# Kernel optimization log

Measured on AMD Instinct MI355X. Metric: run time of the kernel, lower is better.

Reference implementation:

```python
import jax, jax.numpy as jnp
import numpy as np

N, E = 50000, 800000
C, H, EC = 64, 3, 32  # node_channels, heads, edge_channels
NEG_SLOPE = 0.2


def _kaiming(key, shape, fan_in):
    bound = np.sqrt(6.0 / fan_in)  # kaiming_uniform_ default (a=sqrt(5)-ish approx; gain sqrt(2) variant)
    return jax.random.uniform(key, shape, jnp.float32, -bound, bound)


def setup_inputs() -> dict:
    key = jax.random.key(0)
    ks = jax.random.split(key, 8)
    x = jax.random.normal(ks[0], (N, C), jnp.float32)
    edge_index = jax.random.randint(ks[1], (2, E), 0, N, jnp.int64)
    edge_attr = jax.random.normal(ks[2], (E, EC), jnp.float32)
    weight_node = _kaiming(ks[3], (C, H * C), C)
    weight_edge = _kaiming(ks[4], (EC, H * C), EC)
    weight_triplet_att = _kaiming(ks[5], (1, H, 3 * C), 3 * C)
    weight_scale = _kaiming(ks[6], (H * C, C), H * C)
    bias = jnp.zeros((C,), jnp.float32)
    return {"x": x, "edge_index": edge_index, "edge_attr": edge_attr,
            "weight_node": weight_node, "weight_edge": weight_edge,
            "weight_triplet_att": weight_triplet_att,
            "weight_scale": weight_scale, "bias": bias}


def reference(x, edge_index, edge_attr, weight_node, weight_edge,
              weight_triplet_att, weight_scale, bias):
    src = edge_index[0]  # j (source)
    dst = edge_index[1]  # i (target), PyG default flow source_to_target

    xp = x @ weight_node                     # [N, H*C]
    ep = edge_attr @ weight_edge             # [E, H*C]

    x_j = xp[src].reshape(E, H, C)
    x_i = xp[dst].reshape(E, H, C)
    e_ij = ep.reshape(E, H, C)

    # attention weight split along concat order [x_i, e_ij, x_j]
    w = weight_triplet_att.reshape(H, 3, C)
    alpha = (jnp.einsum('ehc,hc->eh', x_i, w[:, 0])
             + jnp.einsum('ehc,hc->eh', e_ij, w[:, 1])
             + jnp.einsum('ehc,hc->eh', x_j, w[:, 2]))   # [E, H]
    alpha = jnp.where(alpha >= 0, alpha, NEG_SLOPE * alpha)  # leaky_relu

    # segment softmax over destination nodes (PyG softmax semantics)
    seg_max = jax.ops.segment_max(alpha, dst, num_segments=N)    # [N, H]
    alpha = jnp.exp(alpha - seg_max[dst])
    seg_sum = jax.ops.segment_sum(alpha, dst, num_segments=N)    # [N, H]
    alpha = alpha / (seg_sum[dst] + 1e-16)

    msg = alpha[:, :, None] * e_ij * x_j                         # [E, H, C]
    aggr = jax.ops.segment_sum(msg.reshape(E, H * C), dst, num_segments=N)  # [N, H*C]

    return aggr @ weight_scale + bias                            # [N, C]
```

## Files before the change

kernel.cpp:

```cpp
#include <hip/hip_runtime.h>

#define CC    64
#define HH    3
#define ECC   32
#define HCdim 192
#define NEG_SLOPE 0.2f
#define ASHIFT 12.0f

typedef float v2f __attribute__((ext_vector_type(2)));

__global__ void tm_k0(const float* __restrict__ We, const float* __restrict__ wt,
                      float* __restrict__ u) {
    int t = threadIdx.x;
    if (t >= HH * ECC) return;
    int h = t >> 5, k = t & 31;
    float s = 0.f;
    #pragma unroll
    for (int c = 0; c < CC; ++c)
        s = fmaf(We[k * HCdim + h * CC + c], wt[h * HCdim + CC + c], s);
    u[t] = s;
}

#define K1_ROWS 64
__global__ __launch_bounds__(192) void tm_k1(const float* __restrict__ x,
        const float* __restrict__ Wn, const float* __restrict__ wt,
        const int* __restrict__ ei, int* __restrict__ deg,
        float* __restrict__ xp, float* __restrict__ sA, int N, int E) {
    __shared__ float wl[CC * HCdim];
    __shared__ float xl[K1_ROWS * CC];
    const int t = threadIdx.x;
    for (int i = blockIdx.x * 192 + t; i < E; i += gridDim.x * 192)
        atomicAdd(&deg[ei[E + i]], 1);
    const int h = t >> 6, c = t & 63;
    {
        float4* wl4 = (float4*)wl;
        const float4* Wn4 = (const float4*)Wn;
        for (int i = t; i < CC * HCdim / 4; i += 192) wl4[i] = Wn4[i];
    }
    const int base = blockIdx.x * K1_ROWS;
    const int rows = min(K1_ROWS, N - base);
    {
        float4* xl4 = (float4*)xl;
        const float4* x4 = (const float4*)(x + (size_t)base * CC);
        for (int i = t; i < rows * CC / 4; i += 192) xl4[i] = x4[i];
    }
    const float w0c = wt[h * HCdim + c];
    const float w2c = wt[h * HCdim + 2 * CC + c];
    __syncthreads();
    for (int rt = 0; rt < rows; rt += 4) {
        float acc0 = 0.f, acc1 = 0.f, acc2 = 0.f, acc3 = 0.f;
        #pragma unroll 4
        for (int k = 0; k < CC; k += 4) {
            const float w0  = wl[(k + 0) * HCdim + t];
            const float w1  = wl[(k + 1) * HCdim + t];
            const float w2_ = wl[(k + 2) * HCdim + t];
            const float w3  = wl[(k + 3) * HCdim + t];
            const float4 xa = *(const float4*)&xl[(rt + 0) * CC + k];
            const float4 xb = *(const float4*)&xl[(rt + 1) * CC + k];
            const float4 xc = *(const float4*)&xl[(rt + 2) * CC + k];
            const float4 xd = *(const float4*)&xl[(rt + 3) * CC + k];
            acc0 = fmaf(xa.x, w0, fmaf(xa.y, w1, fmaf(xa.z, w2_, fmaf(xa.w, w3, acc0))));
            acc1 = fmaf(xb.x, w0, fmaf(xb.y, w1, fmaf(xb.z, w2_, fmaf(xb.w, w3, acc1))));
            acc2 = fmaf(xc.x, w0, fmaf(xc.y, w1, fmaf(xc.z, w2_, fmaf(xc.w, w3, acc2))));
            acc3 = fmaf(xd.x, w0, fmaf(xd.y, w1, fmaf(xd.z, w2_, fmaf(xd.w, w3, acc3))));
        }
        #pragma unroll
        for (int r = 0; r < 4; ++r) {
            const float v = (r == 0) ? acc0 : (r == 1) ? acc1 : (r == 2) ? acc2 : acc3;
            const int n = base + rt + r;
            xp[(size_t)n * HCdim + t] = v;
            float a0 = v * w0c, a2 = v * w2c;
            #pragma unroll
            for (int o = 32; o; o >>= 1) {
                a0 += __shfl_xor(a0, o);
                a2 += __shfl_xor(a2, o);
            }
            if (c == 0) {
                sA[n * 8 + h]     = a0;
                sA[n * 8 + 4 + h] = a2;
            }
        }
    }
}

__global__ __launch_bounds__(256) void tm_scanA(const int* __restrict__ deg,
        int* __restrict__ bsum, int N) {
    __shared__ int sd[256];
    int t = threadIdx.x, n = blockIdx.x * 256 + t;
    sd[t] = (n < N) ? deg[n] : 0;
    __syncthreads();
    for (int o = 128; o; o >>= 1) {
        if (t < o) sd[t] += sd[t + o];
        __syncthreads();
    }
    if (!t) bsum[blockIdx.x] = sd[0];
}

__global__ __launch_bounds__(256) void tm_scanB(const int* __restrict__ bsum,
        int* __restrict__ boff, int nb) {
    __shared__ int sd[256];
    int t = threadIdx.x;
    int v = (t < nb) ? bsum[t] : 0;
    sd[t] = v;
    __syncthreads();
    for (int o = 1; o < 256; o <<= 1) {
        int x = (t >= o) ? sd[t - o] : 0;
        __syncthreads();
        sd[t] += x;
        __syncthreads();
    }
    if (t < nb) boff[t] = sd[t] - v;
}

__global__ __launch_bounds__(256) void tm_scanC(const int* __restrict__ deg,
        const int* __restrict__ boff, int* __restrict__ off,
        int* __restrict__ cursor, int N) {
    __shared__ int sd[256];
    int t = threadIdx.x, n = blockIdx.x * 256 + t;
    int v = (n < N) ? deg[n] : 0;
    sd[t] = v;
    __syncthreads();
    for (int o = 1; o < 256; o <<= 1) {
        int x = (t >= o) ? sd[t - o] : 0;
        __syncthreads();
        sd[t] += x;
        __syncthreads();
    }
    if (n < N) {
        int ex = boff[blockIdx.x] + sd[t] - v;
        off[n] = ex;
        cursor[n] = ex;
        if (n == N - 1) off[N] = ex + v;
    }
}

__global__ __launch_bounds__(256) void tm_alpha(const int* __restrict__ ei,
        const float* __restrict__ ea, const float* __restrict__ u,
        const float* __restrict__ sA, int* __restrict__ cursor,
        float4* __restrict__ alphaE, int2* __restrict__ perm, int E) {
    __shared__ float ul[HH * ECC];
    const int t = threadIdx.x;
    if (t < HH * ECC) ul[t] = u[t];
    __syncthreads();
    const int e = blockIdx.x * 256 + t;
    if (e >= E) return;
    const int src = ei[e];
    const int dst = ei[E + e];
    float av[ECC];
    const float4* p4 = (const float4*)(ea + (size_t)e * ECC);
    #pragma unroll
    for (int q = 0; q < 8; ++q) {
        float4 v = p4[q];
        av[4*q] = v.x; av[4*q+1] = v.y; av[4*q+2] = v.z; av[4*q+3] = v.w;
    }
    float d0 = 0.f, d1 = 0.f, d2 = 0.f;
    #pragma unroll
    for (int k = 0; k < ECC; ++k) {
        d0 = fmaf(av[k], ul[k], d0);
        d1 = fmaf(av[k], ul[ECC + k], d1);
        d2 = fmaf(av[k], ul[2 * ECC + k], d2);
    }
    const float4 s0 = *(const float4*)(sA + (size_t)dst * 8);
    const float4 s2 = *(const float4*)(sA + (size_t)src * 8 + 4);
    float a0 = s0.x + d0 + s2.x;
    float a1 = s0.y + d1 + s2.y;
    float a2 = s0.z + d2 + s2.z;
    a0 = (a0 >= 0.f) ? a0 : NEG_SLOPE * a0;
    a1 = (a1 >= 0.f) ? a1 : NEG_SLOPE * a1;
    a2 = (a2 >= 0.f) ? a2 : NEG_SLOPE * a2;
    alphaE[e] = make_float4(a0, a1, a2, 0.f);
    const int pos = atomicAdd(&cursor[dst], 1);
    perm[pos] = make_int2(src * (HCdim * 4), e * (ECC * 4));
}

__global__ __launch_bounds__(192) void tm_agg(const int2* __restrict__ perm,
        const int* __restrict__ off, const float* __restrict__ ea,
        const float* __restrict__ We, const float* __restrict__ alphaE,
        const float* __restrict__ xp, float* __restrict__ aggrN, int N) {
    const int t = threadIdx.x;
    const int h = t >> 6, lane = t & 63;
    const char* __restrict__ ea_b = (const char*)ea;
    const char* __restrict__ xp_b = (const char*)xp;
    const char* __restrict__ al_b = (const char*)alphaE;
    v2f wcol2[16];
    #pragma unroll
    for (int k2 = 0; k2 < 16; ++k2) {
        wcol2[k2].x = We[(2 * k2)     * HCdim + h * CC + lane];
        wcol2[k2].y = We[(2 * k2 + 1) * HCdim + h * CC + lane];
    }
    const int xoff = h * CC * 4 + lane * 4;
    const int aoff = h * 4;
    for (int n = blockIdx.x; n < N; n += gridDim.x) {
        const int start = off[n], end = off[n + 1];
        float s = 0.f, acc = 0.f;
        int pos = start;
        for (; pos + 2 <= end; pos += 2) {
            const int4 pp = *(const int4*)&perm[pos];
            const int so0 = __builtin_amdgcn_readfirstlane(pp.x);
            const int eo0 = __builtin_amdgcn_readfirstlane(pp.y);
            const int so1 = __builtin_amdgcn_readfirstlane(pp.z);
            const int eo1 = __builtin_amdgcn_readfirstlane(pp.w);
            const float a0 = *(const float*)(al_b + (eo0 >> 3) + aoff);
            const float a1 = *(const float*)(al_b + (eo1 >> 3) + aoff);
            const float4* q0 = (const float4*)(ea_b + eo0);
            const float4* q1 = (const float4*)(ea_b + eo1);
            const float xj0 = *(const float*)(xp_b + so0 + xoff);
            const float xj1 = *(const float*)(xp_b + so1 + xoff);
            v2f d0 = {0.f, 0.f}, d1 = {0.f, 0.f};
            #pragma unroll
            for (int q = 0; q < 8; ++q) {
                const float4 v0 = q0[q];
                const float4 v1 = q1[q];
                const v2f wlo = wcol2[2 * q], whi = wcol2[2 * q + 1];
                d0 = (v2f){v0.x, v0.y} * wlo + d0;
                d0 = (v2f){v0.z, v0.w} * whi + d0;
                d1 = (v2f){v1.x, v1.y} * wlo + d1;
                d1 = (v2f){v1.z, v1.w} * whi + d1;
            }
            const float p0 = __expf(a0 - ASHIFT);
            const float p1 = __expf(a1 - ASHIFT);
            s += p0 + p1;
            acc = fmaf(p0 * (d0.x + d0.y), xj0, acc);
            acc = fmaf(p1 * (d1.x + d1.y), xj1, acc);
        }
        if (pos < end) {
            const int2 pe = perm[pos];
            const int so = __builtin_amdgcn_readfirstlane(pe.x);
            const int eo = __builtin_amdgcn_readfirstlane(pe.y);
            const float a = *(const float*)(al_b + (eo >> 3) + aoff);
            const float4* q4 = (const float4*)(ea_b + eo);
            const float xj = *(const float*)(xp_b + so + xoff);
            v2f d = {0.f, 0.f};
            #pragma unroll
            for (int q = 0; q < 8; ++q) {
                const float4 v = q4[q];
                d = (v2f){v.x, v.y} * wcol2[2 * q]     + d;
                d = (v2f){v.z, v.w} * wcol2[2 * q + 1] + d;
            }
            const float p = __expf(a - ASHIFT);
            s += p;
            acc = fmaf(p * (d.x + d.y), xj, acc);
        }
        aggrN[(size_t)n * HCdim + h * CC + lane] = acc / (s + 1e-16f);
    }
}

#define K5_ROWS 16
__global__ __launch_bounds__(256) void tm_k5(const float* __restrict__ aggrN,
        const float* __restrict__ Ws, const float* __restrict__ bias,
        float* __restrict__ out, int N) {
    __shared__ float wsl[HCdim * CC];
    __shared__ float al[K5_ROWS * HCdim];
    const int t = threadIdx.x;
    const int part = t >> 6, c = t & 63;
    {
        float4* w4 = (float4*)wsl;
        const float4* Ws4 = (const float4*)Ws;
        for (int i = t; i < HCdim * CC / 4; i += 256) w4[i] = Ws4[i];
    }
    const float b = bias[c];
    const int base = blockIdx.x * K5_ROWS;
    const int rows = min(K5_ROWS, N - base);
    {
        float4* al4 = (float4*)al;
        const float4* a4 = (const float4*)(aggrN + (size_t)base * HCdim);
        for (int i = t; i < rows * HCdim / 4; i += 256) al4[i] = a4[i];
    }
    __syncthreads();
    const int r0 = part * 4;
    if (r0 >= rows) return;
    float acc0 = b, acc1 = b, acc2 = b, acc3 = b;
    #pragma unroll 4
    for (int k = 0; k < HCdim; k += 4) {
        const float w0  = wsl[(k + 0) * CC + c];
        const float w1  = wsl[(k + 1) * CC + c];
        const float w2_ = wsl[(k + 2) * CC + c];
        const float w3  = wsl[(k + 3) * CC + c];
        const float4 xa = *(const float4*)&al[(r0 + 0) * HCdim + k];
        const float4 xb = *(const float4*)&al[(r0 + 1) * HCdim + k];
        const float4 xc = *(const float4*)&al[(r0 + 2) * HCdim + k];
        const float4 xd = *(const float4*)&al[(r0 + 3) * HCdim + k];
        acc0 = fmaf(xa.x, w0, fmaf(xa.y, w1, fmaf(xa.z, w2_, fmaf(xa.w, w3, acc0))));
        acc1 = fmaf(xb.x, w0, fmaf(xb.y, w1, fmaf(xb.z, w2_, fmaf(xb.w, w3, acc1))));
        acc2 = fmaf(xc.x, w0, fmaf(xc.y, w1, fmaf(xc.z, w2_, fmaf(xc.w, w3, acc2))));
        acc3 = fmaf(xd.x, w0, fmaf(xd.y, w1, fmaf(xd.z, w2_, fmaf(xd.w, w3, acc3))));
    }
    if (r0 + 0 < rows) out[(size_t)(base + r0 + 0) * CC + c] = acc0;
    if (r0 + 1 < rows) out[(size_t)(base + r0 + 1) * CC + c] = acc1;
    if (r0 + 2 < rows) out[(size_t)(base + r0 + 2) * CC + c] = acc2;
    if (r0 + 3 < rows) out[(size_t)(base + r0 + 3) * CC + c] = acc3;
}

extern "C" void kernel_launch(void* const* d_in, const int* in_sizes, int n_in,
                              void* d_out, int out_size, void* d_ws, size_t ws_size,
                              hipStream_t stream) {
    const float* x    = (const float*)d_in[0];
    const int*   ei   = (const int*)d_in[1];
    const float* ea   = (const float*)d_in[2];
    const float* Wn   = (const float*)d_in[3];
    const float* We   = (const float*)d_in[4];
    const float* wt   = (const float*)d_in[5];
    const float* Ws   = (const float*)d_in[6];
    const float* bias = (const float*)d_in[7];
    float* out = (float*)d_out;
    const int N = in_sizes[0] / CC;
    const int E = in_sizes[1] / 2;
    const int nb = (N + 255) / 256;

    float* ws = (float*)d_ws;
    size_t o = 0;
    float* xp = ws + o;                  o += (size_t)N * HCdim;
    float* sA = ws + o;                  o += (size_t)N * 8;
    float* u  = ws + o;                  o += 128;
    float4* alphaE = (float4*)(ws + o);  o += (size_t)E * 4;
    int2*  perm = (int2*)(ws + o);       o += (size_t)E * 2 + 32;
    int* deg    = (int*)(ws + o);        o += N;
    int* off    = (int*)(ws + o);        o += N + 1;
    int* cursor = (int*)(ws + o);        o += N;
    int* bsum   = (int*)(ws + o);        o += 256;
    int* boff   = (int*)(ws + o);        o += 256;
    o += (4 - (o & 3)) & 3;
    float* aggrN = ws + o;               o += (size_t)N * HCdim;
    (void)ws_size; (void)n_in; (void)out_size;

    (void)hipMemsetAsync(deg, 0, (size_t)N * sizeof(int), stream);

    tm_k0<<<1, 96, 0, stream>>>(We, wt, u);
    tm_k1<<<(N + K1_ROWS - 1) / K1_ROWS, 192, 0, stream>>>(x, Wn, wt, ei, deg,
                                                           xp, sA, N, E);
    tm_scanA<<<nb, 256, 0, stream>>>(deg, bsum, N);
    tm_scanB<<<1, 256, 0, stream>>>(bsum, boff, nb);
    tm_scanC<<<nb, 256, 0, stream>>>(deg, boff, off, cursor, N);
    tm_alpha<<<(E + 255) / 256, 256, 0, stream>>>(ei, ea, u, sA, cursor,
                                                  alphaE, perm, E);
    tm_agg<<<(N + 7) / 8, 192, 0, stream>>>(perm, off, ea, We,
                                            (const float*)alphaE, xp, aggrN, N);
    tm_k5<<<(N + K5_ROWS - 1) / K5_ROWS, 256, 0, stream>>>(aggrN, Ws, bias, out, N);
}
```

Before: 437.1 us.

## Store projected node features in fp16 and prefetch edge permutation in aggregation

The node projection xp is written as half precision, which halves the bytes of the random per-edge gather of x_j in the aggregation kernel and halves the xp write traffic. Alpha is pre-shifted and pre-scaled by log2(e) when written, so aggregation can use exp2 directly. The perm pair load is software-pipelined one iteration ahead. The cost is reduced precision in x_j, which could affect accuracy tolerance.

```diff
diff --git a/kernel.cpp b/kernel.cpp
--- a/kernel.cpp
+++ b/kernel.cpp
@@ -6,6 +6,7 @@
 #define HCdim 192
 #define NEG_SLOPE 0.2f
 #define ASHIFT 12.0f
+#define LOG2E  1.44269504f
 
 typedef float v2f __attribute__((ext_vector_type(2)));
 
@@ -25,7 +26,7 @@
 __global__ __launch_bounds__(192) void tm_k1(const float* __restrict__ x,
         const float* __restrict__ Wn, const float* __restrict__ wt,
         const int* __restrict__ ei, int* __restrict__ deg,
-        float* __restrict__ xp, float* __restrict__ sA, int N, int E) {
+        _Float16* __restrict__ xp16, float* __restrict__ sA, int N, int E) {
     __shared__ float wl[CC * HCdim];
     __shared__ float xl[K1_ROWS * CC];
     const int t = threadIdx.x;
@@ -68,7 +69,7 @@
         for (int r = 0; r < 4; ++r) {
             const float v = (r == 0) ? acc0 : (r == 1) ? acc1 : (r == 2) ? acc2 : acc3;
             const int n = base + rt + r;
-            xp[(size_t)n * HCdim + t] = v;
+            xp16[(size_t)n * HCdim + t] = (_Float16)v;
             float a0 = v * w0c, a2 = v * w2c;
             #pragma unroll
             for (int o = 32; o; o >>= 1) {
@@ -168,19 +169,21 @@
     a0 = (a0 >= 0.f) ? a0 : NEG_SLOPE * a0;
     a1 = (a1 >= 0.f) ? a1 : NEG_SLOPE * a1;
     a2 = (a2 >= 0.f) ? a2 : NEG_SLOPE * a2;
-    alphaE[e] = make_float4(a0, a1, a2, 0.f);
+    alphaE[e] = make_float4((a0 - ASHIFT) * LOG2E,
+                            (a1 - ASHIFT) * LOG2E,
+                            (a2 - ASHIFT) * LOG2E, 0.f);
     const int pos = atomicAdd(&cursor[dst], 1);
-    perm[pos] = make_int2(src * (HCdim * 4), e * (ECC * 4));
+    perm[pos] = make_int2(src * (HCdim * 2), e * (ECC * 4));
 }
 
 __global__ __launch_bounds__(192) void tm_agg(const int2* __restrict__ perm,
         const int* __restrict__ off, const float* __restrict__ ea,
         const float* __restrict__ We, const float* __restrict__ alphaE,
-        const float* __restrict__ xp, float* __restrict__ aggrN, int N) {
+        const _Float16* __restrict__ xp16, float* __restrict__ aggrN, int N) {
     const int t = threadIdx.x;
     const int h = t >> 6, lane = t & 63;
     const char* __restrict__ ea_b = (const char*)ea;
-    const char* __restrict__ xp_b = (const char*)xp;
+    const char* __restrict__ xp_b = (const char*)xp16;
     const char* __restrict__ al_b = (const char*)alphaE;
     v2f wcol2[16];
     #pragma unroll
@@ -188,24 +191,28 @@
         wcol2[k2].x = We[(2 * k2)     * HCdim + h * CC + lane];
         wcol2[k2].y = We[(2 * k2 + 1) * HCdim + h * CC + lane];
     }
-    const int xoff = h * CC * 4 + lane * 4;
+    const int xoff = h * (CC * 2) + lane * 2;
     const int aoff = h * 4;
     for (int n = blockIdx.x; n < N; n += gridDim.x) {
         const int start = off[n], end = off[n + 1];
         float s = 0.f, acc = 0.f;
         int pos = start;
-        for (; pos + 2 <= end; pos += 2) {
-            const int4 pp = *(const int4*)&perm[pos];
-            const int so0 = __builtin_amdgcn_readfirstlane(pp.x);
-            const int eo0 = __builtin_amdgcn_readfirstlane(pp.y);
-            const int so1 = __builtin_amdgcn_readfirstlane(pp.z);
-            const int eo1 = __builtin_amdgcn_readfirstlane(pp.w);
+        int4 pp = (pos + 2 <= end) ? *(const int4*)&perm[pos]
+                                   : make_int4(0, 0, 0, 0);
+        for (; pos + 2 <= end; ) {
+            const int4 cur = pp;
+            pos += 2;
+            if (pos + 2 <= end) pp = *(const int4*)&perm[pos];
+            const int so0 = __builtin_amdgcn_readfirstlane(cur.x);
+            const int eo0 = __builtin_amdgcn_readfirstlane(cur.y);
+            const int so1 = __builtin_amdgcn_readfirstlane(cur.z);
+            const int eo1 = __builtin_amdgcn_readfirstlane(cur.w);
             const float a0 = *(const float*)(al_b + (eo0 >> 3) + aoff);
             const float a1 = *(const float*)(al_b + (eo1 >> 3) + aoff);
             const float4* q0 = (const float4*)(ea_b + eo0);
             const float4* q1 = (const float4*)(ea_b + eo1);
-            const float xj0 = *(const float*)(xp_b + so0 + xoff);
-            const float xj1 = *(const float*)(xp_b + so1 + xoff);
+            const float xj0 = (float)*(const _Float16*)(xp_b + so0 + xoff);
+            const float xj1 = (float)*(const _Float16*)(xp_b + so1 + xoff);
             v2f d0 = {0.f, 0.f}, d1 = {0.f, 0.f};
             #pragma unroll
             for (int q = 0; q < 8; ++q) {
@@ -217,8 +224,8 @@
                 d1 = (v2f){v1.x, v1.y} * wlo + d1;
                 d1 = (v2f){v1.z, v1.w} * whi + d1;
             }
-            const float p0 = __expf(a0 - ASHIFT);
-            const float p1 = __expf(a1 - ASHIFT);
+            const float p0 = exp2f(a0);
+            const float p1 = exp2f(a1);
             s += p0 + p1;
             acc = fmaf(p0 * (d0.x + d0.y), xj0, acc);
             acc = fmaf(p1 * (d1.x + d1.y), xj1, acc);
@@ -229,7 +236,7 @@
             const int eo = __builtin_amdgcn_readfirstlane(pe.y);
             const float a = *(const float*)(al_b + (eo >> 3) + aoff);
             const float4* q4 = (const float4*)(ea_b + eo);
-            const float xj = *(const float*)(xp_b + so + xoff);
+            const float xj = (float)*(const _Float16*)(xp_b + so + xoff);
             v2f d = {0.f, 0.f};
             #pragma unroll
             for (int q = 0; q < 8; ++q) {
@@ -237,7 +244,7 @@
                 d = (v2f){v.x, v.y} * wcol2[2 * q]     + d;
                 d = (v2f){v.z, v.w} * wcol2[2 * q + 1] + d;
             }
-            const float p = __expf(a - ASHIFT);
+            const float p = exp2f(a);
             s += p;
             acc = fmaf(p * (d.x + d.y), xj, acc);
         }
@@ -309,7 +316,7 @@
 
     float* ws = (float*)d_ws;
     size_t o = 0;
-    float* xp = ws + o;                  o += (size_t)N * HCdim;
+    _Float16* xp16 = (_Float16*)(ws + o); o += (size_t)N * HCdim / 2;
     float* sA = ws + o;                  o += (size_t)N * 8;
     float* u  = ws + o;                  o += 128;
     float4* alphaE = (float4*)(ws + o);  o += (size_t)E * 4;
@@ -327,13 +334,13 @@
 
     tm_k0<<<1, 96, 0, stream>>>(We, wt, u);
     tm_k1<<<(N + K1_ROWS - 1) / K1_ROWS, 192, 0, stream>>>(x, Wn, wt, ei, deg,
-                                                           xp, sA, N, E);
+                                                           xp16, sA, N, E);
     tm_scanA<<<nb, 256, 0, stream>>>(deg, bsum, N);
     tm_scanB<<<1, 256, 0, stream>>>(bsum, boff, nb);
     tm_scanC<<<nb, 256, 0, stream>>>(deg, boff, off, cursor, N);
     tm_alpha<<<(E + 255) / 256, 256, 0, stream>>>(ei, ea, u, sA, cursor,
                                                   alphaE, perm, E);
     tm_agg<<<(N + 7) / 8, 192, 0, stream>>>(perm, off, ea, We,
-                                            (const float*)alphaE, xp, aggrN, N);
+                                            (const float*)alphaE, xp16, aggrN, N);
     tm_k5<<<(N + K5_ROWS - 1) / K5_ROWS, 256, 0, stream>>>(aggrN, Ws, bias, out, N);
 }
```

Result: faster. 423.6 us (-3.1%).
